# Performance work log

Measured on AMD Instinct MI355X. Metric: run time of the kernel, lower is better.

The kernel has to match this reference:

```python
import jax, jax.numpy as jnp
import numpy as np

K = 3          # kernel_size
STRIDE = 1
PAD = 1
NUM_BASIS = 8
DEGREE = 3
M = NUM_BASIS + DEGREE   # number of basis slots (11)
EPS = 1e-5               # BatchNorm2d default eps


def _unfold(x):
    # x: [B,C,H,W] -> patches [B,C,L,K*K] (L = Ho*Wo spatial positions, last dim = kernel pos)
    x = jnp.pad(x, ((0, 0), (0, 0), (PAD, PAD), (PAD, PAD)))
    B, C, H, W = x.shape
    Ho = (H - K) // STRIDE + 1
    Wo = (W - K) // STRIDE + 1
    ii = (jnp.arange(Ho) * STRIDE)[:, None] + jnp.arange(K)[None, :]   # [Ho,K]
    jj = (jnp.arange(Wo) * STRIDE)[:, None] + jnp.arange(K)[None, :]   # [Wo,K]
    p = x[:, :, ii[:, None, :, None], jj[None, :, None, :]]           # [B,C,Ho,Wo,K,K]
    return p.reshape(B, C, Ho * Wo, K * K), Ho, Wo


def _bspline_basis(u):
    # Vectorized Cox-de Boor recursion, faithful to the module's in-place update
    # (entries j >= M-d keep their stale lower-degree values, as in the original).
    # u: [...,] in (0,1) -> basis [..., M]
    knots = jnp.linspace(0.0, 1.0, M + 1).astype(u.dtype)              # 12 knots
    b = ((u[..., None] >= knots[:M]) & (u[..., None] < knots[1:M + 1])).astype(u.dtype)
    for d in range(1, DEGREE + 1):
        n = M - d
        j = np.arange(n)
        den1 = knots[j + d] - knots[j]
        den2 = knots[j + d + 1] - knots[j + 1]
        alpha = jnp.where(den1 != 0, (u[..., None] - knots[j]) / jnp.where(den1 != 0, den1, 1.0), 0.0)
        beta = jnp.where(den2 != 0, (knots[j + d + 1] - u[..., None]) / jnp.where(den2 != 0, den2, 1.0), 0.0)
        upd = alpha * b[..., :n] + beta * b[..., 1:n + 1]
        b = jnp.concatenate([upd, b[..., n:]], axis=-1)
    return b


def setup_inputs() -> dict:
    key = jax.random.key(0)
    k1, k2, k3 = jax.random.split(key, 3)
    B, C_in, C_out, H, W = 8, 64, 128, 56, 56
    x = jax.random.normal(k1, (B, C_in, H, W), dtype=jnp.float32)
    # Xavier-uniform-like scale for control points [O, C, K*K, M]
    fan = C_in * K * K * M + C_out
    bound_cp = float(np.sqrt(6.0 / fan))
    control_points = jax.random.uniform(k2, (C_out, C_in, K * K, M), minval=-bound_cp, maxval=bound_cp, dtype=jnp.float32)
    bound_w = float(np.sqrt(6.0 / (C_in * K * K + C_out * K * K)))
    conv_w = jax.random.uniform(k3, (C_out, C_in, K, K), minval=-bound_w, maxval=bound_w, dtype=jnp.float32)
    conv_b = jnp.zeros((C_out,), dtype=jnp.float32)
    bn_gamma = jnp.ones((C_out,), dtype=jnp.float32)
    bn_beta = jnp.zeros((C_out,), dtype=jnp.float32)
    return {"x": x, "control_points": control_points, "conv_w": conv_w,
            "conv_b": conv_b, "bn_gamma": bn_gamma, "bn_beta": bn_beta}


def reference(x, control_points, conv_w, conv_b, bn_gamma, bn_beta):
    patches, Ho, Wo = _unfold(x)                 # [B,C,L,K2]
    u = jax.nn.sigmoid(patches)
    basis = _bspline_basis(u)                    # [B,C,L,K2,M]
    # spline output: contract in_channels, kernel positions, basis index
    spline = jnp.einsum('bclkn,ockn->bol', basis, control_points)
    B = x.shape[0]
    O = control_points.shape[0]
    spline = spline.reshape(B, O, Ho, Wo)
    conv = jax.lax.conv_general_dilated(x, conv_w, (STRIDE, STRIDE), [(PAD, PAD), (PAD, PAD)],
                                        dimension_numbers=('NCHW', 'OIHW', 'NCHW'))
    out = spline + conv + conv_b[None, :, None, None]
    # Dropout2d is identity in eval mode. BatchNorm2d with batch statistics (training default).
    mean = out.mean(axis=(0, 2, 3), keepdims=True)
    var = out.var(axis=(0, 2, 3), keepdims=True)
    out = (out - mean) * jax.lax.rsqrt(var + EPS)
    return out * bn_gamma[None, :, None, None] + bn_beta[None, :, None, None]
```

## Files before the change

kernel.cpp:

```cpp
#include <hip/hip_runtime.h>
#include <math.h>

#define CIN   64
#define COUT  128
#define HW    56
#define L_    3136
#define KTOT  6912
#define TH    8
#define TW    8
#define HALO_W 10
#define NPIX  100
#define CSTR  (NPIX*16 + 32)
#define G8_SIZE (8*CSTR)
#define G4_SIZE (4*CSTR)
#define BUF_SIZE (G8_SIZE+G4_SIZE)

#define BP_BYTES (COUT * KTOT * 2)
#define PART_OFF BP_BYTES
#define SS_OFF   (PART_OFF + 2048 * 4)

typedef __attribute__((ext_vector_type(8))) short bf16x8;
typedef __attribute__((ext_vector_type(4))) float f32x4;
typedef unsigned long long u64;

#define BLOAD(dst, addr) \
    asm volatile("global_load_dwordx4 %0, %1, off" : "=v"(dst) : "v"(addr))
#define XLOAD(dst, addr) \
    asm volatile("global_load_dword %0, %1, off" : "=v"(dst) : "v"(addr))

__device__ __forceinline__ unsigned short f2bf(float f) {
    unsigned int u = __float_as_uint(f);
    return (unsigned short)((u + 0x7FFFu + ((u >> 16) & 1u)) >> 16);
}
__device__ __forceinline__ unsigned int pk2(float a, float b) {
    return (unsigned int)f2bf(a) | ((unsigned int)f2bf(b) << 16);
}

__device__ __forceinline__ void eval_store(float xv, char* g8rec, char* g4half) {
    float u  = 1.0f / (1.0f + __expf(-xv));
    float tt = u * 11.0f;
    int s = (int)floorf(tt);
    s = (s > 10) ? 10 : s;
    float xf  = tt - (float)s;
    float x2  = xf * xf, x3 = x2 * xf;
    float omx = 1.0f - xf;
    const float i6 = 1.0f / 6.0f;
    float w3 = x3 * i6;
    float w2 = fmaf(fmaf(fmaf(-3.0f, xf, 3.0f), xf, 3.0f), xf, 1.0f) * i6;
    float w1 = fmaf(fmaf(3.0f, xf, -6.0f), x2, 4.0f) * i6;
    float w0 = omx * omx * omx * i6;

    unsigned int b0 = f2bf(w0), b1 = f2bf(w1), b2 = f2bf(w2), b3 = f2bf(w3);
    unsigned int slot[8];
#pragma unroll
    for (int j = 0; j < 8; j++) {
        unsigned int v = 0;
        v = (s == j)     ? b3 : v;
        v = (s == j + 1) ? b2 : v;
        v = (s == j + 2) ? b1 : v;
        v = (s == j + 3) ? b0 : v;
        slot[j] = v;
    }
    uint4 rec;
    rec.x = slot[0] | (slot[1] << 16);
    rec.y = slot[2] | (slot[3] << 16);
    rec.z = slot[4] | (slot[5] << 16);
    rec.w = slot[6] | (slot[7] << 16);
    *reinterpret_cast<uint4*>(g8rec) = rec;

    float y = tt - 8.0f;
    float f8 = 0.0f;
    f8 = (s == 8)  ? 0.5f * y * y : f8;
    f8 = (s == 9)  ? 0.5f * fmaf(-2.0f * y, y, fmaf(6.0f, y, -3.0f)) : f8;
    f8 = (s == 10) ? 0.5f * (3.0f - y) * (3.0f - y) : f8;
    float z = tt - 9.0f;
    float f9 = 0.0f;
    f9 = (s == 9)  ? z : f9;
    f9 = (s == 10) ? 2.0f - z : f9;
    float f10 = (s == 10) ? 1.0f : 0.0f;
    *reinterpret_cast<uint2*>(g4half) = make_uint2(pk2(f8, f9), pk2(f10, xv));
}

__global__ __launch_bounds__(256) void k_packB(const float* __restrict__ cp,
                                               const float* __restrict__ w,
                                               unsigned short* __restrict__ Bp) {
    int idx = blockIdx.x * 256 + threadIdx.x;
    if (idx >= COUT * KTOT) return;
    int kstep = idx >> 12;
    int rem   = idx & 4095;
    int o     = rem >> 5;
    int e32   = rem & 31;
    int ch = kstep / 27, sc = kstep - ch * 27;
    int ktap = sc / 3, ph = sc - ktap * 3;
    int c, n;
    if (ph < 2) { c = ch * 8 + ph * 4 + (e32 >> 3); n = e32 & 7; }
    else        { int sub = e32 & 7; c = ch * 8 + (e32 >> 3) * 2 + (sub >> 2); n = 8 + (sub & 3); }
    float v;
    if (n < 11) v = cp[(((size_t)o * CIN + c) * 9 + ktap) * 11 + n];
    else        v = w[((size_t)o * CIN + c) * 9 + ktap];
    Bp[idx] = f2bf(v);
}

__global__ __launch_bounds__(256) void k_main(const float* __restrict__ x,
                                              const unsigned short* __restrict__ Bp,
                                              float* __restrict__ out,
                                              float* __restrict__ part) {
    __shared__ char lds[2 * BUF_SIZE];

    const int bid  = blockIdx.x;
    const int b    = bid & 7;
    const int tile = bid >> 3;
    const int th   = tile / 7;
    const int tw   = tile - th * 7;
    const int t    = threadIdx.x;
    const int lane = t & 63;
    const int wid  = t >> 6;

    const bool valid = (t < 200);
    const int p     = (t < 100) ? t : (t - 100);
    const int hi100 = (t >= 100) ? 1 : 0;
    const int ph_  = p / 10, pw_ = p - ph_ * 10;
    const int hg = th * TH - 1 + ph_;
    const int wg = tw * TW - 1 + pw_;
    const bool inb = valid && (hg >= 0) && (hg < HW) && (wg >= 0) && (wg < HW);
    const u64 xadv = inb ? (u64)8 * L_ * 4 : 0;
    u64 px[4];
#pragma unroll
    for (int r = 0; r < 4; r++) {
        int c0 = 2 * r + hi100;
        px[r] = inb ? ((u64)x + (((u64)b * CIN + c0) * L_ + (u64)hg * HW + wg) * 4)
                    : (u64)x;
    }

    const int q   = lane >> 4;
    const int r15 = lane & 15;
    int P[4];
#pragma unroll
    for (int mi = 0; mi < 4; mi++) {
        int lh = mi * 2 + (r15 >> 3);
        int lw = r15 & 7;
        P[mi] = (lh * HALO_W + lw) * 16 + q * CSTR;
    }
    const int obase = wid * 32 + r15;

    const u64 bend = (u64)Bp + BP_BYTES;
    u64 pa0 = (u64)Bp + ((u64)obase * 64) + ((u64)q * 16);
    u64 pa1 = pa0 + 1024;

    f32x4 acc[4][2];
#pragma unroll
    for (int mi = 0; mi < 4; mi++)
#pragma unroll
        for (int ni = 0; ni < 2; ni++) acc[mi][ni] = (f32x4){0.f, 0.f, 0.f, 0.f};

    float xa[4];
    XLOAD(xa[0], px[0]); XLOAD(xa[1], px[1]);
    XLOAD(xa[2], px[2]); XLOAD(xa[3], px[3]);
#pragma unroll
    for (int r = 0; r < 4; r++) px[r] += xadv;
    asm volatile("s_waitcnt vmcnt(0)");
    __builtin_amdgcn_sched_barrier(0);
    if (valid) {
#pragma unroll
        for (int r = 0; r < 4; r++) {
            float va = inb ? xa[r] : 0.0f;
            int c = 2 * r + hi100;
            eval_store(va, &lds[c * CSTR + p * 16],
                       &lds[G8_SIZE + r * CSTR + p * 16 + hi100 * 8]);
        }
    }
    __syncthreads();

    bf16x8 breg0[9], breg1[9];
#pragma unroll
    for (int s = 0; s < 9; s++) {
        BLOAD(breg0[s], pa0);
        BLOAD(breg1[s], pa1);
        pa0 += 8192; pa1 += 8192;
    }

#pragma unroll 1
    for (int ch = 0; ch < 8; ch++) {
        XLOAD(xa[0], px[0]); XLOAD(xa[1], px[1]);
        XLOAD(xa[2], px[2]); XLOAD(xa[3], px[3]);
        if (ch < 6) {
#pragma unroll
            for (int r = 0; r < 4; r++) px[r] += xadv;
        }

        char* abuf = &lds[(ch & 1) * BUF_SIZE];
        char* nbuf = &lds[((ch + 1) & 1) * BUF_SIZE];

        bf16x8 areg[3][4];
        auto aread = [&](int s, bf16x8 (&a)[4]) {
            int k = s / 3, bp = s - k * 3;
            int ki = k / 3, kj = k - ki * 3;
            int poff = (ki * HALO_W + kj) * 16;
            int aoff = (bp == 2) ? (G8_SIZE + poff) : (bp * 4 * CSTR + poff);
#pragma unroll
            for (int mi = 0; mi < 4; mi++)
                a[mi] = *reinterpret_cast<const bf16x8*>(abuf + P[mi] + aoff);
        };
        aread(0, areg[0]);
        aread(1, areg[1]);

#pragma unroll
        for (int s = 0; s < 27; s++) {
            asm volatile("s_waitcnt vmcnt(16)");
            __builtin_amdgcn_sched_barrier(0);
            const int bs = s % 9;
#pragma unroll
            for (int mi = 0; mi < 4; mi++) {
                acc[mi][0] = __builtin_amdgcn_mfma_f32_16x16x32_bf16(areg[s % 3][mi], breg0[bs], acc[mi][0], 0, 0, 0);
                acc[mi][1] = __builtin_amdgcn_mfma_f32_16x16x32_bf16(areg[s % 3][mi], breg1[bs], acc[mi][1], 0, 0, 0);
            }
            if (s + 2 < 27) aread(s + 2, areg[(s + 2) % 3]);
            BLOAD(breg0[bs], pa0);
            BLOAD(breg1[bs], pa1);
            pa0 += 8192; if (pa0 >= bend) pa0 -= BP_BYTES;
            pa1 += 8192; if (pa1 >= bend) pa1 -= BP_BYTES;
        }

        if (ch < 7 && valid) {
#pragma unroll
            for (int r = 0; r < 4; r++) {
                float va = inb ? xa[r] : 0.0f;
                int c = 2 * r + hi100;
                eval_store(va, &nbuf[c * CSTR + p * 16],
                           &nbuf[G8_SIZE + r * CSTR + p * 16 + hi100 * 8]);
            }
        }
        __syncthreads();
    }

    float psum[2] = {0.f, 0.f}, psq[2] = {0.f, 0.f};
#pragma unroll
    for (int ni = 0; ni < 2; ni++) {
        int o = obase + ni * 16;
#pragma unroll
        for (int mi = 0; mi < 4; mi++) {
            int lh = mi * 2 + (q >> 1);
            int lw0 = (q & 1) * 4;
            int lg = (th * TH + lh) * HW + tw * TW + lw0;
            float4 v;
            v.x = acc[mi][ni][0];
            v.y = acc[mi][ni][1];
            v.z = acc[mi][ni][2];
            v.w = acc[mi][ni][3];
            *reinterpret_cast<float4*>(&out[(size_t)(b * COUT + o) * L_ + lg]) = v;
            psum[ni] += v.x + v.y + v.z + v.w;
            psq[ni]  += v.x * v.x + v.y * v.y + v.z * v.z + v.w * v.w;
        }
    }
#pragma unroll
    for (int ni = 0; ni < 2; ni++) {
        psum[ni] += __shfl_xor(psum[ni], 16);
        psum[ni] += __shfl_xor(psum[ni], 32);
        psq[ni]  += __shfl_xor(psq[ni], 16);
        psq[ni]  += __shfl_xor(psq[ni], 32);
    }
    if (q == 0) {
#pragma unroll
        for (int ni = 0; ni < 2; ni++) {
            int o = obase + ni * 16;
            atomicAdd(&part[b * COUT + o], psum[ni]);
            atomicAdd(&part[1024 + b * COUT + o], psq[ni]);
        }
    }
}

__global__ __launch_bounds__(128) void k_final(const float* __restrict__ part,
                                               const float* __restrict__ gamma,
                                               const float* __restrict__ beta,
                                               float* __restrict__ ss) {
    int o = threadIdx.x;
    float sum = 0.f, sq = 0.f;
#pragma unroll
    for (int b = 0; b < 8; b++) {
        sum += part[b * COUT + o];
        sq  += part[1024 + b * COUT + o];
    }
    float n = (float)(8 * L_);
    float mean = sum / n;
    float var  = sq / n - mean * mean;
    float scale = gamma[o] * rsqrtf(var + 1e-5f);
    ss[o]        = scale;
    ss[COUT + o] = beta[o] - mean * scale;
}

__global__ __launch_bounds__(256) void k_norm(float* __restrict__ out,
                                              const float* __restrict__ ss) {
    const int n4 = 8 * COUT * L_ / 4;
    for (int i = blockIdx.x * 256 + threadIdx.x; i < n4; i += gridDim.x * 256) {
        int o = ((i * 4) / L_) & (COUT - 1);
        float sc = ss[o], sh = ss[COUT + o];
        float4 v = reinterpret_cast<float4*>(out)[i];
        v.x = fmaf(v.x, sc, sh);
        v.y = fmaf(v.y, sc, sh);
        v.z = fmaf(v.z, sc, sh);
        v.w = fmaf(v.w, sc, sh);
        reinterpret_cast<float4*>(out)[i] = v;
    }
}

extern "C" void kernel_launch(void* const* d_in, const int* in_sizes, int n_in,
                              void* d_out, int out_size, void* d_ws, size_t ws_size,
                              hipStream_t stream) {
    const float* x     = (const float*)d_in[0];
    const float* cp    = (const float*)d_in[1];
    const float* w     = (const float*)d_in[2];
    const float* gamma = (const float*)d_in[4];
    const float* beta  = (const float*)d_in[5];
    float* out = (float*)d_out;

    unsigned short* Bp = (unsigned short*)d_ws;
    float* part = (float*)((char*)d_ws + PART_OFF);
    float* ss   = (float*)((char*)d_ws + SS_OFF);

    hipMemsetAsync(part, 0, 2048 * sizeof(float), stream);
    k_packB<<<(COUT * KTOT + 255) / 256, 256, 0, stream>>>(cp, w, Bp);
    k_main<<<8 * 49, 256, 0, stream>>>(x, Bp, out, part);
    k_final<<<1, 128, 0, stream>>>(part, gamma, beta, ss);
    k_norm<<<2048, 256, 0, stream>>>(out, ss);
}
```

Baseline: 82.92 us.

## Switch main GEMM to 32x32x16 bf16 MFMA with 2x2 wave tiling

Replaces the 16x16x32 MFMA tiling (each wave handling 64 pixels by 32 output channels with eight MFMAs per k-step) with 32x32x16 MFMAs. Waves now form a 2x2 grid over 64 pixels by 128 channels, and each wave issues two MFMAs per 16-wide k-step across 54 steps. The B-packing kernel, LDS A-read addressing, B-load strides and the epilogue and reduction are all rewritten to match the new fragment layout. This cuts LDS A-fragment reads per wave and uses the larger MFMA shape. In exchange each B fragment is loaded by two waves instead of one, doubling global B traffic per block, and the prefetch pipeline now has half the k-depth per load.

```diff
diff --git a/kernel.cpp b/kernel.cpp
--- a/kernel.cpp
+++ b/kernel.cpp
@@ -19,8 +19,8 @@
 #define PART_OFF BP_BYTES
 #define SS_OFF   (PART_OFF + 2048 * 4)
 
-typedef __attribute__((ext_vector_type(8))) short bf16x8;
-typedef __attribute__((ext_vector_type(4))) float f32x4;
+typedef __attribute__((ext_vector_type(8)))  short bf16x8;
+typedef __attribute__((ext_vector_type(16))) float f32x16;
 typedef unsigned long long u64;
 
 #define BLOAD(dst, addr) \
@@ -86,12 +86,14 @@
                                                unsigned short* __restrict__ Bp) {
     int idx = blockIdx.x * 256 + threadIdx.x;
     if (idx >= COUT * KTOT) return;
-    int kstep = idx >> 12;
-    int rem   = idx & 4095;
-    int o     = rem >> 5;
-    int e32   = rem & 31;
-    int ch = kstep / 27, sc = kstep - ch * 27;
-    int ktap = sc / 3, ph = sc - ktap * 3;
+    int k16 = idx >> 11;
+    int rem = idx & 2047;
+    int o   = rem >> 4;
+    int e16 = rem & 15;
+    int ch  = k16 / 54, s54 = k16 - ch * 54;
+    int g32 = s54 >> 1, khalf = s54 & 1;
+    int ktap = g32 / 3, ph = g32 - ktap * 3;
+    int e32 = khalf * 16 + e16;
     int c, n;
     if (ph < 2) { c = ch * 8 + ph * 4 + (e32 >> 3); n = e32 & 7; }
     else        { int sub = e32 & 7; c = ch * 8 + (e32 >> 3) * 2 + (sub >> 2); n = 8 + (sub & 3); }
@@ -115,6 +117,8 @@
     const int t    = threadIdx.x;
     const int lane = t & 63;
     const int wid  = t >> 6;
+    const int mh   = wid >> 1;
+    const int om   = wid & 1;
 
     const bool valid = (t < 200);
     const int p     = (t < 100) ? t : (t - 100);
@@ -132,26 +136,22 @@
                     : (u64)x;
     }
 
-    const int q   = lane >> 4;
-    const int r15 = lane & 15;
-    int P[4];
-#pragma unroll
-    for (int mi = 0; mi < 4; mi++) {
-        int lh = mi * 2 + (r15 >> 3);
-        int lw = r15 & 7;
-        P[mi] = (lh * HALO_W + lw) * 16 + q * CSTR;
-    }
-    const int obase = wid * 32 + r15;
+    const int l31 = lane & 31;
+    const int lh5 = lane >> 5;
+    int P0;
+    {
+        int row = mh * 32 + l31;
+        int lh = row >> 3, lw = row & 7;
+        P0 = (lh * HALO_W + lw) * 16 + lh5 * CSTR;
+    }
 
     const u64 bend = (u64)Bp + BP_BYTES;
-    u64 pa0 = (u64)Bp + ((u64)obase * 64) + ((u64)q * 16);
-    u64 pa1 = pa0 + 1024;
-
-    f32x4 acc[4][2];
-#pragma unroll
-    for (int mi = 0; mi < 4; mi++)
-#pragma unroll
-        for (int ni = 0; ni < 2; ni++) acc[mi][ni] = (f32x4){0.f, 0.f, 0.f, 0.f};
+    u64 pa0 = (u64)Bp + (u64)((om * 2 + 0) * 32 + l31) * 32 + (u64)lh5 * 16;
+    u64 pa1 = (u64)Bp + (u64)((om * 2 + 1) * 32 + l31) * 32 + (u64)lh5 * 16;
+
+    f32x16 acc0, acc1;
+#pragma unroll
+    for (int i = 0; i < 16; i++) { acc0[i] = 0.f; acc1[i] = 0.f; }
 
     float xa[4];
     XLOAD(xa[0], px[0]); XLOAD(xa[1], px[1]);
@@ -176,8 +176,10 @@
     for (int s = 0; s < 9; s++) {
         BLOAD(breg0[s], pa0);
         BLOAD(breg1[s], pa1);
-        pa0 += 8192; pa1 += 8192;
-    }
+        pa0 += 4096; pa1 += 4096;
+    }
+
+    bf16x8 areg[3];
 
 #pragma unroll 1
     for (int ch = 0; ch < 8; ch++) {
@@ -191,35 +193,34 @@
         char* abuf = &lds[(ch & 1) * BUF_SIZE];
         char* nbuf = &lds[((ch + 1) & 1) * BUF_SIZE];
 
-        bf16x8 areg[3][4];
-        auto aread = [&](int s, bf16x8 (&a)[4]) {
-            int k = s / 3, bp = s - k * 3;
-            int ki = k / 3, kj = k - ki * 3;
-            int poff = (ki * HALO_W + kj) * 16;
-            int aoff = (bp == 2) ? (G8_SIZE + poff) : (bp * 4 * CSTR + poff);
-#pragma unroll
-            for (int mi = 0; mi < 4; mi++)
-                a[mi] = *reinterpret_cast<const bf16x8*>(abuf + P[mi] + aoff);
-        };
-        aread(0, areg[0]);
-        aread(1, areg[1]);
-
-#pragma unroll
-        for (int s = 0; s < 27; s++) {
+#define AREAD(ss, slot) do { \
+        int g32_ = (ss) >> 1, kh_ = (ss) & 1; \
+        int kt_ = g32_ / 3, ph2_ = g32_ - kt_ * 3; \
+        int ki_ = kt_ / 3, kj_ = kt_ - ki_ * 3; \
+        int poff_ = (ki_ * HALO_W + kj_) * 16; \
+        int aoff_ = (ph2_ == 2) ? (G8_SIZE + (kh_ * 2) * CSTR + poff_) \
+                                : ((ph2_ * 4 + kh_ * 2) * CSTR + poff_); \
+        areg[slot] = *reinterpret_cast<const bf16x8*>(abuf + P0 + aoff_); \
+    } while (0)
+
+        AREAD(0, 0);
+        AREAD(1, 1);
+
+#pragma unroll
+        for (int s = 0; s < 54; s++) {
             asm volatile("s_waitcnt vmcnt(16)");
             __builtin_amdgcn_sched_barrier(0);
             const int bs = s % 9;
-#pragma unroll
-            for (int mi = 0; mi < 4; mi++) {
-                acc[mi][0] = __builtin_amdgcn_mfma_f32_16x16x32_bf16(areg[s % 3][mi], breg0[bs], acc[mi][0], 0, 0, 0);
-                acc[mi][1] = __builtin_amdgcn_mfma_f32_16x16x32_bf16(areg[s % 3][mi], breg1[bs], acc[mi][1], 0, 0, 0);
-            }
-            if (s + 2 < 27) aread(s + 2, areg[(s + 2) % 3]);
+            const int cs = s % 3;
+            acc0 = __builtin_amdgcn_mfma_f32_32x32x16_bf16(areg[cs], breg0[bs], acc0, 0, 0, 0);
+            acc1 = __builtin_amdgcn_mfma_f32_32x32x16_bf16(areg[cs], breg1[bs], acc1, 0, 0, 0);
+            if (s + 2 < 54) AREAD(s + 2, (s + 2) % 3);
             BLOAD(breg0[bs], pa0);
             BLOAD(breg1[bs], pa1);
-            pa0 += 8192; if (pa0 >= bend) pa0 -= BP_BYTES;
-            pa1 += 8192; if (pa1 >= bend) pa1 -= BP_BYTES;
-        }
+            pa0 += 4096; if (pa0 >= bend) pa0 -= BP_BYTES;
+            pa1 += 4096; if (pa1 >= bend) pa1 -= BP_BYTES;
+        }
+#undef AREAD
 
         if (ch < 7 && valid) {
 #pragma unroll
@@ -235,36 +236,35 @@
 
     float psum[2] = {0.f, 0.f}, psq[2] = {0.f, 0.f};
 #pragma unroll
-    for (int ni = 0; ni < 2; ni++) {
-        int o = obase + ni * 16;
-#pragma unroll
-        for (int mi = 0; mi < 4; mi++) {
-            int lh = mi * 2 + (q >> 1);
-            int lw0 = (q & 1) * 4;
+    for (int j = 0; j < 2; j++) {
+        const f32x16& a = j ? acc1 : acc0;
+        int o = (om * 2 + j) * 32 + l31;
+#pragma unroll
+        for (int q4 = 0; q4 < 4; q4++) {
+            int lh  = mh * 4 + q4;
+            int lw0 = 4 * lh5;
             int lg = (th * TH + lh) * HW + tw * TW + lw0;
             float4 v;
-            v.x = acc[mi][ni][0];
-            v.y = acc[mi][ni][1];
-            v.z = acc[mi][ni][2];
-            v.w = acc[mi][ni][3];
+            v.x = a[4 * q4 + 0];
+            v.y = a[4 * q4 + 1];
+            v.z = a[4 * q4 + 2];
+            v.w = a[4 * q4 + 3];
             *reinterpret_cast<float4*>(&out[(size_t)(b * COUT + o) * L_ + lg]) = v;
-            psum[ni] += v.x + v.y + v.z + v.w;
-            psq[ni]  += v.x * v.x + v.y * v.y + v.z * v.z + v.w * v.w;
-        }
-    }
-#pragma unroll
-    for (int ni = 0; ni < 2; ni++) {
-        psum[ni] += __shfl_xor(psum[ni], 16);
-        psum[ni] += __shfl_xor(psum[ni], 32);
-        psq[ni]  += __shfl_xor(psq[ni], 16);
-        psq[ni]  += __shfl_xor(psq[ni], 32);
-    }
-    if (q == 0) {
-#pragma unroll
-        for (int ni = 0; ni < 2; ni++) {
-            int o = obase + ni * 16;
-            atomicAdd(&part[b * COUT + o], psum[ni]);
-            atomicAdd(&part[1024 + b * COUT + o], psq[ni]);
+            psum[j] += v.x + v.y + v.z + v.w;
+            psq[j]  += v.x * v.x + v.y * v.y + v.z * v.z + v.w * v.w;
+        }
+    }
+#pragma unroll
+    for (int j = 0; j < 2; j++) {
+        psum[j] += __shfl_xor(psum[j], 32);
+        psq[j]  += __shfl_xor(psq[j], 32);
+    }
+    if (lh5 == 0) {
+#pragma unroll
+        for (int j = 0; j < 2; j++) {
+            int o = (om * 2 + j) * 32 + l31;
+            atomicAdd(&part[b * COUT + o], psum[j]);
+            atomicAdd(&part[1024 + b * COUT + o], psq[j]);
         }
     }
 }
```

Measured after the change: 90.12 us. +8.7%, slower.
